# Kernel optimization log

Measured on AMD Instinct MI355X. Metric: run time of the kernel, lower is better.

Reference implementation:

```python
import jax, jax.numpy as jnp
import numpy as np

D_MODEL = 2048
D_HEAD = 128
NUM_HEADS = 16
D_KV_LATENT = 512
BATCH = 2
SEQ = 2048


def setup_inputs() -> dict:
    key = jax.random.key(0)
    ks = jax.random.split(key, 6)
    s = 0.02
    return {
        "x": jax.random.normal(ks[0], (BATCH, SEQ, D_MODEL), jnp.float32),
        "Wd": jax.random.normal(ks[1], (D_KV_LATENT, D_MODEL), jnp.float32) * s,
        "Wuk": jax.random.normal(ks[2], (NUM_HEADS * D_HEAD, D_KV_LATENT), jnp.float32) * s,
        "Wuv": jax.random.normal(ks[3], (NUM_HEADS * D_HEAD, D_KV_LATENT), jnp.float32) * s,
        "Wq": jax.random.normal(ks[4], (NUM_HEADS * D_HEAD, D_MODEL), jnp.float32) * s,
        "Wo": jax.random.normal(ks[5], (D_MODEL, NUM_HEADS * D_HEAD), jnp.float32) * s,
        "use_cache": 1,
    }


def _mla_cache_path(x, Wd, Wuk, Wuv, Wq, Wo):
    # Weight-absorbed MLA prefill from an empty cache (total_seq_len == seq_len).
    b, s, dm = x.shape
    h, dh, c = NUM_HEADS, D_HEAD, D_KV_LATENT
    # latents = downsample(x): [b, s, c]
    latents = jnp.einsum("bsm,cm->bsc", x, Wd)
    # absorbed weights: q_uk [h, dm, c], out_uv [h, dm, c]
    q_uk = jnp.einsum("hdm,hdc->hmc", Wq.reshape(h, dh, dm), Wuk.reshape(h, dh, c))
    out_uv = jnp.einsum("mhd,hdc->hmc", Wo.reshape(dm, h, dh), Wuv.reshape(h, dh, c))
    # query_part: [b, h, s, c]
    query_part = jnp.einsum("bsm,hmc->bhsc", x, q_uk)
    # value_part: [b, h, s, dm]
    value_part = jnp.einsum("hmc,btc->bhtm", out_uv, latents)
    # scores over latent dim: [b, h, s, s]
    scores = jnp.einsum("bhsc,btc->bhst", query_part, latents) / np.sqrt(dh).astype(np.float32)
    causal = jnp.triu(jnp.ones((s, s), dtype=bool), k=1)
    scores = jnp.where(causal, -jnp.inf, scores)
    attn = jax.nn.softmax(scores, axis=-1)
    # output already in model dim; sum contributions over heads
    out = jnp.einsum("bhst,bhtm->bsm", attn, value_part)
    return out


def reference(x, Wd, Wuk, Wuv, Wq, Wo, use_cache):
    # use_cache is a static Python int (1 -> weight-absorbed cache path)
    return _mla_cache_path(x, Wd, Wuk, Wuv, Wq, Wo)
```

## Files before the change

kernel.cpp:

```cpp
#include <hip/hip_runtime.h>
#include <hip/hip_bf16.h>

typedef __attribute__((ext_vector_type(8))) short short8x;
typedef __attribute__((ext_vector_type(4))) float f32x4;

__device__ __forceinline__ ushort f2bf(float f){
  union { __hip_bfloat16 b; ushort u; } cvt;
  cvt.b = __float2bfloat16(f);
  return cvt.u;
}

__global__ __launch_bounds__(256) void cvt_kernel(const float* __restrict__ in, ushort* __restrict__ out,
                                                  long n, float scale){
  long i = ((long)blockIdx.x * 256 + threadIdx.x) * 4;
  if (i >= n) return;
  float4 v = *(const float4*)(in + i);
  ushort4 o;
  o.x = f2bf(v.x * scale); o.y = f2bf(v.y * scale); o.z = f2bf(v.z * scale); o.w = f2bf(v.w * scale);
  *(ushort4*)(out + i) = o;
}

template<int OUTBF>
__global__ __launch_bounds__(256, 3)
void gemm_bt(const ushort* __restrict__ A, const ushort* __restrict__ BT, void* __restrict__ Cv,
             int M, int N, int K, int lda, int ldb, int ldc,
             long aZ, long bZ, long cZ, float scale)
{
  __shared__ __align__(16) ushort As[2][128 * 32];
  __shared__ __align__(16) ushort Bs[2][128 * 32];
  const int z = blockIdx.z;
  const ushort* Ab = A + (long)z * aZ;
  const ushort* Bb = BT + (long)z * bZ;
  const int tid = threadIdx.x, lane = tid & 63, w = tid >> 6;
  const int wm = w >> 1, wn = w & 1;
  const int lq = lane & 15, q4 = lane >> 4;

  int lin = blockIdx.x + gridDim.x * blockIdx.y;
  const int cpx = (gridDim.x * gridDim.y) >> 3;
  lin = (lin & 7) * cpx + (lin >> 3);
  const int bx = lin % gridDim.x, by = lin / gridDim.x;

  const long arow = (long)by * 128, brow = (long)bx * 128;
  const int lr = lane >> 2, lc = (lane & 3) * 8;

  const f32x4 z4 = {0.f, 0.f, 0.f, 0.f};
  f32x4 acc[4][4];
#pragma unroll
  for (int i = 0; i < 4; i++)
#pragma unroll
    for (int j = 0; j < 4; j++) acc[i][j] = z4;

  auto stage = [&](int buf, int k0){
#pragma unroll
    for (int is = 0; is < 2; ++is){
      const int rb = is * 64 + w * 16;
      const ushort* ga = Ab + (arow + rb + lr) * (long)lda + k0 + lc;
      const ushort* gb = Bb + (brow + rb + lr) * (long)ldb + k0 + lc;
      __builtin_amdgcn_global_load_lds((const __attribute__((address_space(1))) void*)ga,
                                       (__attribute__((address_space(3))) void*)&As[buf][rb * 32], 16, 0, 0);
      __builtin_amdgcn_global_load_lds((const __attribute__((address_space(1))) void*)gb,
                                       (__attribute__((address_space(3))) void*)&Bs[buf][rb * 32], 16, 0, 0);
    }
  };

  const int nk = K >> 5;
  stage(0, 0);
  for (int kt = 0; kt < nk; ++kt){
    __syncthreads();
    if (kt + 1 < nk) stage((kt + 1) & 1, (kt + 1) * 32);
    const int buf = kt & 1;
    short8x a[4], b[4];
#pragma unroll
    for (int i = 0; i < 4; i++){
      a[i] = *(const short8x*)&As[buf][(wm * 64 + i * 16 + lq) * 32 + q4 * 8];
      b[i] = *(const short8x*)&Bs[buf][(wn * 64 + i * 16 + lq) * 32 + q4 * 8];
    }
#pragma unroll
    for (int i = 0; i < 4; i++)
#pragma unroll
      for (int j = 0; j < 4; j++)
        acc[i][j] = __builtin_amdgcn_mfma_f32_16x16x32_bf16(a[i], b[j], acc[i][j], 0, 0, 0);
  }

  const long crowb = arow + wm * 64;
  const long ccolb = brow + wn * 64;
#pragma unroll
  for (int i = 0; i < 4; i++)
#pragma unroll
    for (int j = 0; j < 4; j++)
#pragma unroll
      for (int r = 0; r < 4; r++){
        const long row = crowb + i * 16 + q4 * 4 + r;
        const long col = ccolb + j * 16 + lq;
        const float v = acc[i][j][r] * scale;
        if (OUTBF) ((ushort*)Cv)[(long)z * cZ + row * ldc + col] = f2bf(v);
        else       ((float*)Cv)[(long)z * cZ + row * ldc + col] = v;
      }
}

__global__ __launch_bounds__(256, 1)
void flash10_kernel(const ushort* __restrict__ q, const ushort* __restrict__ k,
                    const ushort* __restrict__ vT, ushort* __restrict__ attnO)
{
  __shared__ __align__(16) ushort Kb[2][64 * 128];
  __shared__ __align__(16) ushort Vb[2][128 * 64];
  __shared__ __align__(16) ushort Pl[4][4][16][72];

  const int tid = threadIdx.x, lane = tid & 63, w = tid >> 6;
  const int lq = lane & 15, q4 = lane >> 4;

  const int xcd = blockIdx.x & 7;
  const int bh = xcd * 4 + ((blockIdx.x >> 3) & 3);
  const int qb = blockIdx.x >> 5;
  const int b = bh & 1, h = bh >> 1;

  const int nt = (qb + 1) * 4;
  const int wdiag = qb * 4 + w;

  const ushort* kb_ = k + (long)b * 2048 * 2048 + h * 128;
  const ushort* vb_ = vT + (long)h * 128 * 4096 + (long)b * 2048;

  const int krow0 = w * 4 + (lane >> 4);
  const int kg = (lane & 15) ^ (krow0 & 7);
  const ushort* kbase = kb_ + (long)krow0 * 2048 + kg * 8;
  const int kofs0 = w * 512;

  const int drow0 = w * 8 + (lane >> 3);
  const int vg = (lane & 7) ^ (drow0 & 7);
  const ushort* vbase = vb_ + (long)drow0 * 4096 + vg * 8;
  const int vofs0 = w * 512;

  auto stage = [&](int buf, int tt){
    const ushort* kp = kbase + (long)tt * 64 * 2048;
    const ushort* vp = vbase + (long)tt * 64;
#pragma unroll
    for (int is = 0; is < 4; ++is){
      __builtin_amdgcn_global_load_lds((const __attribute__((address_space(1))) void*)(kp + (long)is * 16 * 2048),
          (__attribute__((address_space(3))) void*)&Kb[buf][kofs0 + is * 2048], 16, 0, 0);
      __builtin_amdgcn_global_load_lds((const __attribute__((address_space(1))) void*)(vp + (long)is * 32 * 4096),
          (__attribute__((address_space(3))) void*)&Vb[buf][vofs0 + is * 2048], 16, 0, 0);
    }
  };

  const f32x4 z4 = {0.f, 0.f, 0.f, 0.f};

  const int qrow0 = qb * 256 + w * 64;
  const long qgbase = (long)b * 2048 + qrow0;

  short8x qf[4][4];
#pragma unroll
  for (int si = 0; si < 4; si++){
    const ushort* qp = q + (qgbase + si * 16 + lq) * 2560 + h * 128 + q4 * 8;
#pragma unroll
    for (int ks = 0; ks < 4; ks++) qf[si][ks] = *(const short8x*)(qp + ks * 32);
  }

  f32x4 oacc[8][4];
#pragma unroll
  for (int dt = 0; dt < 8; dt++)
#pragma unroll
    for (int si = 0; si < 4; si++) oacc[dt][si] = z4;
  float dsum[4] = {0.f, 0.f, 0.f, 0.f};

  stage(0, 0);
  stage(1, 1);

#pragma unroll 1
  for (int tt = 0; tt < nt; ++tt){
    if (tt == nt - 1) asm volatile("s_waitcnt vmcnt(0)" ::: "memory");
    else              asm volatile("s_waitcnt vmcnt(8)" ::: "memory");
    __syncthreads();
    const int cur = tt & 1;

    if (tt <= wdiag){
      const bool diag = (tt == wdiag);
#pragma unroll
      for (int ti = 0; ti < 4; ++ti){
        const int r = ti * 16 + lq;
        const int rb = r * 128;
        const int rx = r & 7;
        const short8x a0 = *(const short8x*)&Kb[cur][rb + (((q4) ^ rx) * 8)];
        const short8x a1 = *(const short8x*)&Kb[cur][rb + (((4 + q4) ^ rx) * 8)];
        const short8x a2 = *(const short8x*)&Kb[cur][rb + (((8 + q4) ^ rx) * 8)];
        const short8x a3 = *(const short8x*)&Kb[cur][rb + (((12 + q4) ^ rx) * 8)];
#pragma unroll
        for (int si = 0; si < 4; ++si){
          f32x4 st = __builtin_amdgcn_mfma_f32_16x16x32_bf16(a0, qf[si][0], z4, 0, 0, 0);
          st = __builtin_amdgcn_mfma_f32_16x16x32_bf16(a1, qf[si][1], st, 0, 0, 0);
          st = __builtin_amdgcn_mfma_f32_16x16x32_bf16(a2, qf[si][2], st, 0, 0, 0);
          st = __builtin_amdgcn_mfma_f32_16x16x32_bf16(a3, qf[si][3], st, 0, 0, 0);
          ushort4 pb;
#pragma unroll
          for (int r4 = 0; r4 < 4; ++r4){
            const int tl = ti * 16 + q4 * 4 + r4;
            float p = exp2f(st[r4]);
            if (diag && tl > si * 16 + lq) p = 0.f;
            dsum[si] += p;
            ((ushort*)&pb)[r4] = f2bf(p);
          }
          *(ushort4*)&Pl[w][si][lq][ti * 16 + q4 * 4] = pb;
        }
      }
      asm volatile("s_waitcnt lgkmcnt(0)" ::: "memory");
      __builtin_amdgcn_sched_barrier(0);
#pragma unroll
      for (int sp = 0; sp < 2; ++sp){
        const short8x pf00 = *(const short8x*)&Pl[w][2 * sp][lq][q4 * 8];
        const short8x pf01 = *(const short8x*)&Pl[w][2 * sp][lq][32 + q4 * 8];
        const short8x pf10 = *(const short8x*)&Pl[w][2 * sp + 1][lq][q4 * 8];
        const short8x pf11 = *(const short8x*)&Pl[w][2 * sp + 1][lq][32 + q4 * 8];
#pragma unroll
        for (int dt = 0; dt < 8; ++dt){
          const int r = dt * 16 + lq;
          const int rb = r * 64;
          const int rx = lq & 7;
          const short8x av0 = *(const short8x*)&Vb[cur][rb + (((q4) ^ rx) * 8)];
          const short8x av1 = *(const short8x*)&Vb[cur][rb + (((4 + q4) ^ rx) * 8)];
          oacc[dt][2 * sp]     = __builtin_amdgcn_mfma_f32_16x16x32_bf16(av0, pf00, oacc[dt][2 * sp], 0, 0, 0);
          oacc[dt][2 * sp]     = __builtin_amdgcn_mfma_f32_16x16x32_bf16(av1, pf01, oacc[dt][2 * sp], 0, 0, 0);
          oacc[dt][2 * sp + 1] = __builtin_amdgcn_mfma_f32_16x16x32_bf16(av0, pf10, oacc[dt][2 * sp + 1], 0, 0, 0);
          oacc[dt][2 * sp + 1] = __builtin_amdgcn_mfma_f32_16x16x32_bf16(av1, pf11, oacc[dt][2 * sp + 1], 0, 0, 0);
        }
      }
    }
    __syncthreads();
    if (tt + 2 < nt) stage(cur, tt + 2);
  }

  float inv[4];
#pragma unroll
  for (int si = 0; si < 4; ++si){
    float d = dsum[si];
    d += __shfl_xor(d, 16);
    d += __shfl_xor(d, 32);
    inv[si] = 1.f / d;
  }

#pragma unroll
  for (int dt = 0; dt < 8; dt++)
#pragma unroll
    for (int si = 0; si < 4; si++){
      ushort4 o;
      o.x = f2bf(oacc[dt][si][0] * inv[si]);
      o.y = f2bf(oacc[dt][si][1] * inv[si]);
      o.z = f2bf(oacc[dt][si][2] * inv[si]);
      o.w = f2bf(oacc[dt][si][3] * inv[si]);
      *(ushort4*)(attnO + (qgbase + si * 16 + lq) * 2048 + h * 128 + dt * 16 + q4 * 4) = o;
    }
}

extern "C" void kernel_launch(void* const* d_in, const int* in_sizes, int n_in,
                              void* d_out, int out_size, void* d_ws, size_t ws_size,
                              hipStream_t stream)
{
  const float* x   = (const float*)d_in[0];
  const float* Wd  = (const float*)d_in[1];
  const float* Wuk = (const float*)d_in[2];
  const float* Wuv = (const float*)d_in[3];
  const float* Wq  = (const float*)d_in[4];
  const float* Wo  = (const float*)d_in[5];
  float* out = (float*)d_out;
  ushort* ws = (ushort*)d_ws;

  ushort* xb    = ws + 0L;
  ushort* wqdb  = ws + 8388608L;
  ushort* wob   = ws + 13631488L;
  ushort* wukb  = ws + 17825792L;
  ushort* wuvb  = ws + 18874368L;
  ushort* qlat  = ws + 19922944L;
  ushort* kb    = ws + 30408704L;
  ushort* vTb   = ws + 38797312L;
  ushort* attnO = ws + 47185920L;

  const float QSCL = 0.12751744800f;

  cvt_kernel<<<8192, 256, 0, stream>>>(x,   xb,            8388608L, 1.0f);
  cvt_kernel<<<4096, 256, 0, stream>>>(Wq,  wqdb,          4194304L, QSCL);
  cvt_kernel<<<1024, 256, 0, stream>>>(Wd,  wqdb + 4194304L, 1048576L, 1.0f);
  cvt_kernel<<<4096, 256, 0, stream>>>(Wo,  wob,           4194304L, 1.0f);
  cvt_kernel<<<1024, 256, 0, stream>>>(Wuk, wukb,          1048576L, 1.0f);
  cvt_kernel<<<1024, 256, 0, stream>>>(Wuv, wuvb,          1048576L, 1.0f);

  gemm_bt<1><<<dim3(20, 32, 1), 256, 0, stream>>>(xb, wqdb, qlat, 4096, 2560, 2048,
      2048, 2048, 2560, 0L, 0L, 0L, 1.0f);
  gemm_bt<1><<<dim3(16, 32, 1), 256, 0, stream>>>(qlat + 2048, wukb, kb, 4096, 2048, 512,
      2560, 512, 2048, 0L, 0L, 0L, 1.0f);
  gemm_bt<1><<<dim3(32, 16, 1), 256, 0, stream>>>(wuvb, qlat + 2048, vTb, 2048, 4096, 512,
      512, 2560, 4096, 0L, 0L, 0L, 1.0f);
  flash10_kernel<<<256, 256, 0, stream>>>(qlat, kb, vTb, attnO);
  gemm_bt<0><<<dim3(16, 32, 1), 256, 0, stream>>>(attnO, wob, out, 4096, 2048, 2048,
      2048, 2048, 2048, 0L, 0L, 0L, 1.0f);
}
```

Measured before the change: 271.6 us.

## Halve flash query tile to 128 rows, double grid, reorder long strips first

The attention kernel now gives each block a 128-row query strip (32 rows per wave) instead of 256 rows, so the grid doubles to 512 blocks. Strips are ordered so the longest causal strips launch first, which should balance load across CUs and reduce the tail. The P scratch buffer in LDS is also shrunk and XOR-swizzled in place of padding, to avoid bank conflicts. In exchange, each K/V tile loaded into LDS is reused by fewer query rows, which raises total K/V traffic.

```diff
diff --git a/kernel.cpp b/kernel.cpp
--- a/kernel.cpp
+++ b/kernel.cpp
@@ -99,23 +99,28 @@
 }
 
 __global__ __launch_bounds__(256, 1)
-void flash10_kernel(const ushort* __restrict__ q, const ushort* __restrict__ k,
+void flash12_kernel(const ushort* __restrict__ q, const ushort* __restrict__ k,
                     const ushort* __restrict__ vT, ushort* __restrict__ attnO)
 {
   __shared__ __align__(16) ushort Kb[2][64 * 128];
   __shared__ __align__(16) ushort Vb[2][128 * 64];
-  __shared__ __align__(16) ushort Pl[4][4][16][72];
+  __shared__ __align__(16) ushort Pl[4][2][16][64];
 
   const int tid = threadIdx.x, lane = tid & 63, w = tid >> 6;
   const int lq = lane & 15, q4 = lane >> 4;
 
-  const int xcd = blockIdx.x & 7;
-  const int bh = xcd * 4 + ((blockIdx.x >> 3) & 3);
-  const int qb = blockIdx.x >> 5;
+  const int i = blockIdx.x;
+  const int pr = i >> 8;
+  const int ii = i & 255;
+  const int xcd = ii & 7;
+  const int bh = xcd * 4 + ((ii >> 3) & 3);
+  const int j = ii >> 5;
+  const int strip = pr ? j : (15 - j);
   const int b = bh & 1, h = bh >> 1;
 
-  const int nt = (qb + 1) * 4;
-  const int wdiag = qb * 4 + w;
+  const int nt = 2 * (strip + 1);
+  const int wdiag = strip * 2 + (w >> 1);
+  const int moff = (w & 1) * 32;
 
   const ushort* kb_ = k + (long)b * 2048 * 2048 + h * 128;
   const ushort* vb_ = vT + (long)h * 128 * 4096 + (long)b * 2048;
@@ -144,23 +149,23 @@
 
   const f32x4 z4 = {0.f, 0.f, 0.f, 0.f};
 
-  const int qrow0 = qb * 256 + w * 64;
+  const int qrow0 = strip * 128 + w * 32;
   const long qgbase = (long)b * 2048 + qrow0;
 
-  short8x qf[4][4];
-#pragma unroll
-  for (int si = 0; si < 4; si++){
+  short8x qf[2][4];
+#pragma unroll
+  for (int si = 0; si < 2; si++){
     const ushort* qp = q + (qgbase + si * 16 + lq) * 2560 + h * 128 + q4 * 8;
 #pragma unroll
     for (int ks = 0; ks < 4; ks++) qf[si][ks] = *(const short8x*)(qp + ks * 32);
   }
 
-  f32x4 oacc[8][4];
-#pragma unroll
-  for (int dt = 0; dt < 8; dt++)
-#pragma unroll
-    for (int si = 0; si < 4; si++) oacc[dt][si] = z4;
-  float dsum[4] = {0.f, 0.f, 0.f, 0.f};
+  f32x4 oacc[8][2];
+#pragma unroll
+  for (int dt = 0; dt < 8; dt++){ oacc[dt][0] = z4; oacc[dt][1] = z4; }
+  float dsum[2] = {0.f, 0.f};
+
+  const int prx = lq & 7;
 
   stage(0, 0);
   stage(1, 1);
@@ -183,8 +188,10 @@
         const short8x a1 = *(const short8x*)&Kb[cur][rb + (((4 + q4) ^ rx) * 8)];
         const short8x a2 = *(const short8x*)&Kb[cur][rb + (((8 + q4) ^ rx) * 8)];
         const short8x a3 = *(const short8x*)&Kb[cur][rb + (((12 + q4) ^ rx) * 8)];
-#pragma unroll
-        for (int si = 0; si < 4; ++si){
+        const int cG = (ti * 2 + (q4 >> 1)) ^ prx;
+        const int pco = cG * 8 + (q4 & 1) * 4;
+#pragma unroll
+        for (int si = 0; si < 2; ++si){
           f32x4 st = __builtin_amdgcn_mfma_f32_16x16x32_bf16(a0, qf[si][0], z4, 0, 0, 0);
           st = __builtin_amdgcn_mfma_f32_16x16x32_bf16(a1, qf[si][1], st, 0, 0, 0);
           st = __builtin_amdgcn_mfma_f32_16x16x32_bf16(a2, qf[si][2], st, 0, 0, 0);
@@ -194,42 +201,40 @@
           for (int r4 = 0; r4 < 4; ++r4){
             const int tl = ti * 16 + q4 * 4 + r4;
             float p = exp2f(st[r4]);
-            if (diag && tl > si * 16 + lq) p = 0.f;
+            if (diag && tl > moff + si * 16 + lq) p = 0.f;
             dsum[si] += p;
             ((ushort*)&pb)[r4] = f2bf(p);
           }
-          *(ushort4*)&Pl[w][si][lq][ti * 16 + q4 * 4] = pb;
+          *(ushort4*)&Pl[w][si][lq][pco] = pb;
         }
       }
       asm volatile("s_waitcnt lgkmcnt(0)" ::: "memory");
       __builtin_amdgcn_sched_barrier(0);
-#pragma unroll
-      for (int sp = 0; sp < 2; ++sp){
-        const short8x pf00 = *(const short8x*)&Pl[w][2 * sp][lq][q4 * 8];
-        const short8x pf01 = *(const short8x*)&Pl[w][2 * sp][lq][32 + q4 * 8];
-        const short8x pf10 = *(const short8x*)&Pl[w][2 * sp + 1][lq][q4 * 8];
-        const short8x pf11 = *(const short8x*)&Pl[w][2 * sp + 1][lq][32 + q4 * 8];
-#pragma unroll
-        for (int dt = 0; dt < 8; ++dt){
-          const int r = dt * 16 + lq;
-          const int rb = r * 64;
-          const int rx = lq & 7;
-          const short8x av0 = *(const short8x*)&Vb[cur][rb + (((q4) ^ rx) * 8)];
-          const short8x av1 = *(const short8x*)&Vb[cur][rb + (((4 + q4) ^ rx) * 8)];
-          oacc[dt][2 * sp]     = __builtin_amdgcn_mfma_f32_16x16x32_bf16(av0, pf00, oacc[dt][2 * sp], 0, 0, 0);
-          oacc[dt][2 * sp]     = __builtin_amdgcn_mfma_f32_16x16x32_bf16(av1, pf01, oacc[dt][2 * sp], 0, 0, 0);
-          oacc[dt][2 * sp + 1] = __builtin_amdgcn_mfma_f32_16x16x32_bf16(av0, pf10, oacc[dt][2 * sp + 1], 0, 0, 0);
-          oacc[dt][2 * sp + 1] = __builtin_amdgcn_mfma_f32_16x16x32_bf16(av1, pf11, oacc[dt][2 * sp + 1], 0, 0, 0);
-        }
+      const short8x pf00 = *(const short8x*)&Pl[w][0][lq][(q4 ^ prx) * 8];
+      const short8x pf01 = *(const short8x*)&Pl[w][0][lq][((4 + q4) ^ prx) * 8];
+      const short8x pf10 = *(const short8x*)&Pl[w][1][lq][(q4 ^ prx) * 8];
+      const short8x pf11 = *(const short8x*)&Pl[w][1][lq][((4 + q4) ^ prx) * 8];
+      __builtin_amdgcn_sched_barrier(0);
+#pragma unroll
+      for (int dt = 0; dt < 8; ++dt){
+        const int r = dt * 16 + lq;
+        const int rb = r * 64;
+        const int rx = lq & 7;
+        const short8x av0 = *(const short8x*)&Vb[cur][rb + (((q4) ^ rx) * 8)];
+        const short8x av1 = *(const short8x*)&Vb[cur][rb + (((4 + q4) ^ rx) * 8)];
+        oacc[dt][0] = __builtin_amdgcn_mfma_f32_16x16x32_bf16(av0, pf00, oacc[dt][0], 0, 0, 0);
+        oacc[dt][0] = __builtin_amdgcn_mfma_f32_16x16x32_bf16(av1, pf01, oacc[dt][0], 0, 0, 0);
+        oacc[dt][1] = __builtin_amdgcn_mfma_f32_16x16x32_bf16(av0, pf10, oacc[dt][1], 0, 0, 0);
+        oacc[dt][1] = __builtin_amdgcn_mfma_f32_16x16x32_bf16(av1, pf11, oacc[dt][1], 0, 0, 0);
       }
     }
     __syncthreads();
     if (tt + 2 < nt) stage(cur, tt + 2);
   }
 
-  float inv[4];
-#pragma unroll
-  for (int si = 0; si < 4; ++si){
+  float inv[2];
+#pragma unroll
+  for (int si = 0; si < 2; ++si){
     float d = dsum[si];
     d += __shfl_xor(d, 16);
     d += __shfl_xor(d, 32);
@@ -239,7 +244,7 @@
 #pragma unroll
   for (int dt = 0; dt < 8; dt++)
 #pragma unroll
-    for (int si = 0; si < 4; si++){
+    for (int si = 0; si < 2; si++){
       ushort4 o;
       o.x = f2bf(oacc[dt][si][0] * inv[si]);
       o.y = f2bf(oacc[dt][si][1] * inv[si]);
@@ -287,7 +292,7 @@
       2560, 512, 2048, 0L, 0L, 0L, 1.0f);
   gemm_bt<1><<<dim3(32, 16, 1), 256, 0, stream>>>(wuvb, qlat + 2048, vTb, 2048, 4096, 512,
       512, 2560, 4096, 0L, 0L, 0L, 1.0f);
-  flash10_kernel<<<256, 256, 0, stream>>>(qlat, kb, vTb, attnO);
+  flash12_kernel<<<512, 256, 0, stream>>>(qlat, kb, vTb, attnO);
   gemm_bt<0><<<dim3(16, 32, 1), 256, 0, stream>>>(attnO, wob, out, 4096, 2048, 2048,
       2048, 2048, 2048, 0L, 0L, 0L, 1.0f);
 }
```

Result: faster. 237.8 us (-12.5%).
